# Optimization experiments

Measured on AMD Instinct MI355X. Metric: run time of the kernel, lower is better.

The kernel has to match this reference:

```python
import jax, jax.numpy as jnp
import numpy as np

N, D, H, C, E, ED, HID = 50000, 160, 5, 32, 800000, 16, 512
EPS = 1e-5  # torch LayerNorm default
NEG_SLOPE = 0.2  # GATv2Conv default negative_slope


def layer_norm(x, g, b):
    mu = x.mean(-1, keepdims=True)
    var = x.var(-1, keepdims=True)  # biased, matches torch LayerNorm
    return (x - mu) * jax.lax.rsqrt(var + EPS) * g + b


def setup_inputs() -> dict:
    key = jax.random.key(0)
    ks = jax.random.split(key, 12)
    p = lambda k, shape: jax.random.normal(k, shape, jnp.float32) * 0.05
    z = lambda *s: jnp.zeros(s, jnp.float32)
    o = lambda *s: jnp.ones(s, jnp.float32)
    return {
        "x": jax.random.normal(ks[0], (N, D), jnp.float32),
        "edge_index": jax.random.randint(ks[1], (2, E), 0, N),
        "edge_attr": jax.random.normal(ks[2], (E, ED), jnp.float32),
        "u": jax.random.normal(ks[3], (1024, 64), jnp.float32),
        "batch": jax.random.randint(ks[4], (N,), 0, 1024),
        # GATv2Conv params (lin_l, lin_r, lin_edge, att, bias)
        "Wl": p(ks[5], (D, H * C)), "bl": z(H * C),
        "Wr": p(ks[6], (D, H * C)), "br": z(H * C),
        "We": p(ks[7], (ED, H * C)),
        "att": p(ks[8], (H, C)),
        "b_gat": z(H * C),
        # norm1
        "g1": o(D), "b1": z(D),
        # output MLP: Linear(D,HID) -> SELU -> LayerNorm(HID) -> Linear(HID,D)
        "W_m1": p(ks[9], (D, HID)), "b_m1": z(HID),
        "g_m": o(HID), "b_m": z(HID),
        "W_m2": p(ks[10], (HID, D)), "b_m2": z(D),
        # norm2
        "g2": o(D), "b2": z(D),
    }


def reference(x, edge_index, edge_attr, u, batch, Wl, bl, Wr, br, We, att, b_gat,
              g1, b1, W_m1, b_m1, g_m, b_m, W_m2, b_m2, g2, b2):
    src, dst = edge_index[0], edge_index[1]  # messages flow src -> dst
    xl = (x @ Wl + bl).reshape(N, H, C)      # source projection
    xr = (x @ Wr + br).reshape(N, H, C)      # target projection
    ea = (edge_attr @ We).reshape(E, H, C)
    # GATv2 scoring: att . leaky_relu(x_l[j] + x_r[i] + e_ij)
    e = jax.nn.leaky_relu(xl[src] + xr[dst] + ea, NEG_SLOPE)   # [E,H,C]
    score = jnp.einsum('ehc,hc->eh', e, att)                   # [E,H]
    # segment softmax over incoming edges of each target node
    mx = jax.ops.segment_max(score, dst, num_segments=N)       # [N,H]
    ex = jnp.exp(score - mx[dst])
    denom = jax.ops.segment_sum(ex, dst, num_segments=N)
    alpha = ex / denom[dst]                                    # [E,H]
    agg = jax.ops.segment_sum(alpha[:, :, None] * xl[src], dst, num_segments=N)
    attn = agg.reshape(N, H * C) + b_gat                       # concat heads
    # residual + norm, MLP, residual + norm (dropout=0)
    out = layer_norm(x + attn, g1, b1)
    h = layer_norm(jax.nn.selu(out @ W_m1 + b_m1), g_m, b_m)
    mlp = h @ W_m2 + b_m2
    return layer_norm(out + mlp, g2, b2)
```

## Files before the change

kernel.cpp:

```cpp
#include <hip/hip_runtime.h>
#include <math.h>

#define N_NODES 50000
#define D 160
#define H 5
#define C 32
#define HC 160
#define E_EDGES 800000
#define ED 16
#define HID 512
#define EPS 1e-5f
#define NEG_SLOPE 0.2f

typedef __attribute__((ext_vector_type(8))) short bf16x8;
typedef __attribute__((ext_vector_type(4))) float f32x4;
typedef __attribute__((ext_vector_type(4))) short short4v;

__device__ inline float bf2f(short s) {
  unsigned u = ((unsigned)(unsigned short)s) << 16;
  return __builtin_bit_cast(float, u);
}
__device__ inline short f2bf(float f) {
  unsigned u = __builtin_bit_cast(unsigned, f);
  u = u + 0x7fffu + ((u >> 16) & 1u);
  return (short)(u >> 16);
}
__device__ inline float selu_f(float v) {
  return 1.0507009873554805f * (v > 0.f ? v : 1.6732632423543772f * (__expf(v) - 1.f));
}

__global__ void prep_weights(const float* __restrict__ Wl, const float* __restrict__ Wr,
                             const float* __restrict__ Wm1, const float* __restrict__ Wm2,
                             short* __restrict__ WlT, short* __restrict__ WrT,
                             short* __restrict__ W1T, short* __restrict__ W2T) {
  int i = blockIdx.x * blockDim.x + threadIdx.x;
  if (i < 25600) { int n = i / 160, k = i % 160; WlT[n*160 + k] = f2bf(Wl[k*160 + n]); return; }
  i -= 25600;
  if (i < 25600) { int n = i / 160, k = i % 160; WrT[n*160 + k] = f2bf(Wr[k*160 + n]); return; }
  i -= 25600;
  if (i < 81920) { int n = i / 160, k = i % 160; W1T[n*160 + k] = f2bf(Wm1[k*512 + n]); return; }
  i -= 81920;
  if (i < 81920) { int n = i / 512, k = i % 512; W2T[n*512 + k] = f2bf(Wm2[k*160 + n]); return; }
}

__global__ void convert_x(const float* __restrict__ x, short* __restrict__ xb) {
  int i = blockIdx.x * blockDim.x + threadIdx.x;
  if (i < N_NODES * D / 8) {
    const float4* s = (const float4*)(x + (size_t)i * 8);
    float4 a = s[0], b = s[1];
    bf16x8 o;
    o[0] = f2bf(a.x); o[1] = f2bf(a.y); o[2] = f2bf(a.z); o[3] = f2bf(a.w);
    o[4] = f2bf(b.x); o[5] = f2bf(b.y); o[6] = f2bf(b.z); o[7] = f2bf(b.w);
    *(bf16x8*)(xb + (size_t)i * 8) = o;
  }
}

__global__ __launch_bounds__(256) void proj_mfma(
    const short* __restrict__ xb, const short* __restrict__ WlT, const short* __restrict__ WrT,
    const float* __restrict__ bl, const float* __restrict__ br,
    short* __restrict__ xl, short* __restrict__ xr)
{
  __shared__ short As[64][40];
  int t = threadIdx.x;
  int wave = t >> 6, lane = t & 63;
  int lq = lane >> 4, lc = lane & 15;
  int row0 = blockIdx.x * 64;
  f32x4 accl[10] = {}, accr[10] = {};
  for (int kt = 0; kt < 5; ++kt) {
    int k0 = kt * 32;
    {
      int r = t >> 2, seg = t & 3;
      int gr = min(row0 + r, N_NODES - 1);
      bf16x8 v = *(const bf16x8*)&xb[(size_t)gr * 160 + k0 + seg * 8];
      *(bf16x8*)&As[r][seg * 8] = v;
    }
    __syncthreads();
    bf16x8 af = *(bf16x8*)&As[wave * 16 + lc][lq * 8];
#pragma unroll
    for (int ct = 0; ct < 10; ++ct) {
      int cc = ct * 16 + lc;
      bf16x8 bfl = *(const bf16x8*)&WlT[cc * 160 + k0 + lq * 8];
      accl[ct] = __builtin_amdgcn_mfma_f32_16x16x32_bf16(af, bfl, accl[ct], 0, 0, 0);
      bf16x8 bfr = *(const bf16x8*)&WrT[cc * 160 + k0 + lq * 8];
      accr[ct] = __builtin_amdgcn_mfma_f32_16x16x32_bf16(af, bfr, accr[ct], 0, 0, 0);
    }
    __syncthreads();
  }
#pragma unroll
  for (int ct = 0; ct < 10; ++ct) {
    int col = ct * 16 + lc;
    float bbl = bl[col], bbr = br[col];
#pragma unroll
    for (int rg = 0; rg < 4; ++rg) {
      int row = row0 + wave * 16 + lq * 4 + rg;
      if (row < N_NODES) {
        xl[(size_t)row * 160 + col] = f2bf(accl[ct][rg] + bbl);
        xr[(size_t)row * 160 + col] = f2bf(accr[ct][rg] + bbr);
      }
    }
  }
}

__global__ void count_kernel(const int* __restrict__ ei, int* __restrict__ cnt) {
  int e = blockIdx.x * blockDim.x + threadIdx.x;
  if (e < E_EDGES) atomicAdd(&cnt[ei[E_EDGES + e]], 1);
}

__global__ __launch_bounds__(1024) void scan_kernel(const int* __restrict__ cnt,
                                                    int* __restrict__ offs) {
  const int PER = (N_NODES + 1023) / 1024;
  int t = threadIdx.x;
  int start = t * PER;
  int sum = 0;
  for (int i = 0; i < PER; ++i) {
    int idx = start + i;
    if (idx < N_NODES) sum += cnt[idx];
  }
  int lane = t & 63, wid = t >> 6;
  int v = sum;
  for (int off = 1; off < 64; off <<= 1) {
    int u = __shfl_up(v, off, 64);
    if (lane >= off) v += u;
  }
  __shared__ int wsums[16];
  if (lane == 63) wsums[wid] = v;
  __syncthreads();
  if (wid == 0) {
    int w = (lane < 16) ? wsums[lane] : 0;
    for (int off = 1; off < 16; off <<= 1) {
      int u = __shfl_up(w, off, 64);
      if (lane >= off) w += u;
    }
    if (lane < 16) wsums[lane] = w;
  }
  __syncthreads();
  int excl = v - sum + (wid > 0 ? wsums[wid - 1] : 0);
  int run = excl;
  for (int i = 0; i < PER; ++i) {
    int idx = start + i;
    if (idx < N_NODES) { offs[idx] = run; run += cnt[idx]; }
  }
  if (t == 1023) offs[N_NODES] = run;
}

__global__ void scatter2(const int* __restrict__ ei, const float* __restrict__ eattr,
                         const int* __restrict__ offs, int* __restrict__ cursor,
                         int* __restrict__ srcs, short* __restrict__ eacsr) {
  int e = blockIdx.x * blockDim.x + threadIdx.x;
  if (e < E_EDGES) {
    int dst = ei[E_EDGES + e];
    int src = ei[e];
    int slot = atomicAdd(&cursor[dst], 1);
    int j = offs[dst] + slot;
    srcs[j] = src;
    const float4* s = (const float4*)&eattr[(size_t)e * ED];
    float4 v0 = s[0], v1 = s[1], v2 = s[2], v3 = s[3];
    short* o = eacsr + (size_t)j * ED;
    short4v w0, w1, w2, w3;
    w0[0]=f2bf(v0.x); w0[1]=f2bf(v0.y); w0[2]=f2bf(v0.z); w0[3]=f2bf(v0.w);
    w1[0]=f2bf(v1.x); w1[1]=f2bf(v1.y); w1[2]=f2bf(v1.z); w1[3]=f2bf(v1.w);
    w2[0]=f2bf(v2.x); w2[1]=f2bf(v2.y); w2[2]=f2bf(v2.z); w2[3]=f2bf(v2.w);
    w3[0]=f2bf(v3.x); w3[1]=f2bf(v3.y); w3[2]=f2bf(v3.z); w3[3]=f2bf(v3.w);
    *(short4v*)(o + 0) = w0; *(short4v*)(o + 4) = w1;
    *(short4v*)(o + 8) = w2; *(short4v*)(o + 12) = w3;
  }
}

__global__ __launch_bounds__(160) void attn_kernel(
    const short* __restrict__ eacsr, const int* __restrict__ srcs,
    const short* __restrict__ xl, const short* __restrict__ xr,
    const float* __restrict__ x, const float* __restrict__ We,
    const float* __restrict__ att, const float* __restrict__ b_gat,
    const float* __restrict__ g1, const float* __restrict__ b1,
    const int* __restrict__ offs,
    float* __restrict__ outb, short* __restrict__ outb_bf)
{
  __shared__ float sWe[ED][HC];
  int i = blockIdx.x;
  int t = threadIdx.x;
  for (int k = 0; k < ED; ++k) sWe[k][t] = We[k*HC + t];
  float a_t = att[t];
  float xr_t = bf2f(xr[(size_t)i*HC + t]);
  int e0 = offs[i], e1 = offs[i+1];
  __syncthreads();
  float agg = 0.f, denom = 0.f;
  for (int j = e0; j < e1; ++j) {
    int src = srcs[j];
    bf16x8 ev0 = *(const bf16x8*)&eacsr[(size_t)j*ED];
    bf16x8 ev1 = *(const bf16x8*)&eacsr[(size_t)j*ED + 8];
    float ea = 0.f;
#pragma unroll
    for (int k = 0; k < 8; ++k) ea += bf2f(ev0[k]) * sWe[k][t];
#pragma unroll
    for (int k = 0; k < 8; ++k) ea += bf2f(ev1[k]) * sWe[k+8][t];
    float xlv = bf2f(xl[(size_t)src*HC + t]);
    float v = xlv + xr_t + ea;
    v = v > 0.f ? v : NEG_SLOPE*v;
    float p = a_t * v;
#pragma unroll
    for (int m = 16; m >= 1; m >>= 1) p += __shfl_xor(p, m, 32);
    float ex = __expf(p);
    denom += ex;
    agg += ex * xlv;
  }
  float attn = (denom > 0.f) ? agg/denom : 0.f;
  float val = x[(size_t)i*HC + t] + attn + b_gat[t];
  float s1 = val, s2 = val*val;
#pragma unroll
  for (int m = 16; m >= 1; m >>= 1) { s1 += __shfl_xor(s1, m, 32); s2 += __shfl_xor(s2, m, 32); }
  __shared__ float gs1[5], gs2[5];
  __shared__ float smu, srstd;
  if ((t & 31) == 0) { gs1[t>>5] = s1; gs2[t>>5] = s2; }
  __syncthreads();
  if (t == 0) {
    float a = 0.f, b = 0.f;
    for (int g = 0; g < 5; ++g) { a += gs1[g]; b += gs2[g]; }
    float mu = a/160.f, var = b/160.f - mu*mu;
    smu = mu; srstd = rsqrtf(var + EPS);
  }
  __syncthreads();
  float o = (val - smu)*srstd*g1[t] + b1[t];
  outb[(size_t)i*HC + t] = o;
  outb_bf[(size_t)i*HC + t] = f2bf(o);
}

__global__ __launch_bounds__(256) void mlp1_mfma(
    const short* __restrict__ ab, const short* __restrict__ W1T,
    const float* __restrict__ b1m, const float* __restrict__ gm, const float* __restrict__ bm,
    short* __restrict__ h)
{
  __shared__ short As[32][40];
  __shared__ float ps1[4][32], ps2[4][32];
  int t = threadIdx.x;
  int wave = t >> 6, lane = t & 63;
  int lq = lane >> 4, lc = lane & 15;
  int row0 = blockIdx.x * 32;
  f32x4 acc[2][8] = {};
  for (int kt = 0; kt < 5; ++kt) {
    int k0 = kt * 32;
    if (t < 128) {
      int r = t >> 2, seg = t & 3;
      int gr = min(row0 + r, N_NODES - 1);
      bf16x8 v = *(const bf16x8*)&ab[(size_t)gr * 160 + k0 + seg * 8];
      *(bf16x8*)&As[r][seg * 8] = v;
    }
    __syncthreads();
    bf16x8 af0 = *(bf16x8*)&As[lc][lq * 8];
    bf16x8 af1 = *(bf16x8*)&As[16 + lc][lq * 8];
#pragma unroll
    for (int ct = 0; ct < 8; ++ct) {
      int cc = wave * 128 + ct * 16 + lc;
      bf16x8 bfv = *(const bf16x8*)&W1T[cc * 160 + k0 + lq * 8];
      acc[0][ct] = __builtin_amdgcn_mfma_f32_16x16x32_bf16(af0, bfv, acc[0][ct], 0, 0, 0);
      acc[1][ct] = __builtin_amdgcn_mfma_f32_16x16x32_bf16(af1, bfv, acc[1][ct], 0, 0, 0);
    }
    __syncthreads();
  }
  float s1[2][4] = {}, s2[2][4] = {};
#pragma unroll
  for (int rt = 0; rt < 2; ++rt)
#pragma unroll
    for (int ct = 0; ct < 8; ++ct)
#pragma unroll
      for (int rg = 0; rg < 4; ++rg) {
        int cc = wave * 128 + ct * 16 + lc;
        float v = selu_f(acc[rt][ct][rg] + b1m[cc]);
        acc[rt][ct][rg] = v;
        s1[rt][rg] += v; s2[rt][rg] += v * v;
      }
#pragma unroll
  for (int m = 1; m <= 8; m <<= 1) {
#pragma unroll
    for (int rt = 0; rt < 2; ++rt)
#pragma unroll
      for (int rg = 0; rg < 4; ++rg) {
        s1[rt][rg] += __shfl_xor(s1[rt][rg], m, 64);
        s2[rt][rg] += __shfl_xor(s2[rt][rg], m, 64);
      }
  }
  if (lc == 0) {
#pragma unroll
    for (int rt = 0; rt < 2; ++rt)
#pragma unroll
      for (int rg = 0; rg < 4; ++rg) {
        ps1[wave][rt * 16 + lq * 4 + rg] = s1[rt][rg];
        ps2[wave][rt * 16 + lq * 4 + rg] = s2[rt][rg];
      }
  }
  __syncthreads();
  float mu[2][4], rstd[2][4];
#pragma unroll
  for (int rt = 0; rt < 2; ++rt)
#pragma unroll
    for (int rg = 0; rg < 4; ++rg) {
      int rl = rt * 16 + lq * 4 + rg;
      float a = ps1[0][rl] + ps1[1][rl] + ps1[2][rl] + ps1[3][rl];
      float b = ps2[0][rl] + ps2[1][rl] + ps2[2][rl] + ps2[3][rl];
      float m_ = a * (1.f / 512.f);
      float var = b * (1.f / 512.f) - m_ * m_;
      mu[rt][rg] = m_; rstd[rt][rg] = rsqrtf(var + EPS);
    }
#pragma unroll
  for (int rt = 0; rt < 2; ++rt)
#pragma unroll
    for (int ct = 0; ct < 8; ++ct)
#pragma unroll
      for (int rg = 0; rg < 4; ++rg) {
        int row = row0 + rt * 16 + lq * 4 + rg;
        int cc = wave * 128 + ct * 16 + lc;
        if (row < N_NODES)
          h[(size_t)row * 512 + cc] =
              f2bf((acc[rt][ct][rg] - mu[rt][rg]) * rstd[rt][rg] * gm[cc] + bm[cc]);
      }
}

__global__ __launch_bounds__(256) void mlp2_mfma(
    const short* __restrict__ hb, const short* __restrict__ W2T,
    const float* __restrict__ b2m, const float* __restrict__ outb,
    const float* __restrict__ g2, const float* __restrict__ b2,
    float* __restrict__ y)
{
  __shared__ short As[64][40];
  int t = threadIdx.x;
  int wave = t >> 6, lane = t & 63;
  int lq = lane >> 4, lc = lane & 15;
  int row0 = blockIdx.x * 64;
  f32x4 acc[10] = {};
  for (int kt = 0; kt < 16; ++kt) {
    int k0 = kt * 32;
    {
      int r = t >> 2, seg = t & 3;
      int gr = min(row0 + r, N_NODES - 1);
      bf16x8 v = *(const bf16x8*)&hb[(size_t)gr * 512 + k0 + seg * 8];
      *(bf16x8*)&As[r][seg * 8] = v;
    }
    __syncthreads();
    bf16x8 af = *(bf16x8*)&As[wave * 16 + lc][lq * 8];
#pragma unroll
    for (int ct = 0; ct < 10; ++ct) {
      int cc = ct * 16 + lc;
      bf16x8 bfv = *(const bf16x8*)&W2T[cc * 512 + k0 + lq * 8];
      acc[ct] = __builtin_amdgcn_mfma_f32_16x16x32_bf16(af, bfv, acc[ct], 0, 0, 0);
    }
    __syncthreads();
  }
  float s1[4] = {}, s2[4] = {};
#pragma unroll
  for (int ct = 0; ct < 10; ++ct) {
    int col = ct * 16 + lc;
#pragma unroll
    for (int rg = 0; rg < 4; ++rg) {
      int rowl = min(row0 + wave * 16 + lq * 4 + rg, N_NODES - 1);
      float v = acc[ct][rg] + b2m[col] + outb[(size_t)rowl * 160 + col];
      acc[ct][rg] = v;
      s1[rg] += v; s2[rg] += v * v;
    }
  }
#pragma unroll
  for (int m = 1; m <= 8; m <<= 1) {
#pragma unroll
    for (int rg = 0; rg < 4; ++rg) {
      s1[rg] += __shfl_xor(s1[rg], m, 64);
      s2[rg] += __shfl_xor(s2[rg], m, 64);
    }
  }
  float mu[4], rstd[4];
#pragma unroll
  for (int rg = 0; rg < 4; ++rg) {
    float m_ = s1[rg] * (1.f / 160.f);
    float var = s2[rg] * (1.f / 160.f) - m_ * m_;
    mu[rg] = m_; rstd[rg] = rsqrtf(var + EPS);
  }
#pragma unroll
  for (int ct = 0; ct < 10; ++ct) {
    int col = ct * 16 + lc;
#pragma unroll
    for (int rg = 0; rg < 4; ++rg) {
      int row = row0 + wave * 16 + lq * 4 + rg;
      if (row < N_NODES)
        y[(size_t)row * 160 + col] = (acc[ct][rg] - mu[rg]) * rstd[rg] * g2[col] + b2[col];
    }
  }
}

extern "C" void kernel_launch(void* const* d_in, const int* in_sizes, int n_in,
                              void* d_out, int out_size, void* d_ws, size_t ws_size,
                              hipStream_t stream) {
  const float* x     = (const float*)d_in[0];
  const int*   ei    = (const int*)d_in[1];
  const float* eattr = (const float*)d_in[2];
  const float* Wl    = (const float*)d_in[5];
  const float* bl    = (const float*)d_in[6];
  const float* Wr    = (const float*)d_in[7];
  const float* br    = (const float*)d_in[8];
  const float* We    = (const float*)d_in[9];
  const float* att   = (const float*)d_in[10];
  const float* bgat  = (const float*)d_in[11];
  const float* g1    = (const float*)d_in[12];
  const float* b1    = (const float*)d_in[13];
  const float* Wm1   = (const float*)d_in[14];
  const float* bm1   = (const float*)d_in[15];
  const float* gm    = (const float*)d_in[16];
  const float* bm    = (const float*)d_in[17];
  const float* Wm2   = (const float*)d_in[18];
  const float* bm2   = (const float*)d_in[19];
  const float* g2    = (const float*)d_in[20];
  const float* b2    = (const float*)d_in[21];
  float* y = (float*)d_out;

  char* p = (char*)d_ws;
  auto alloc = [&](size_t bytes) {
    void* q = p;
    p += (bytes + 255) & ~(size_t)255;
    return q;
  };
  short* xb      = (short*)alloc((size_t)N_NODES * 160 * 2);
  short* xlb     = (short*)alloc((size_t)N_NODES * 160 * 2);
  short* xrb     = (short*)alloc((size_t)N_NODES * 160 * 2);
  float* outb    = (float*)alloc((size_t)N_NODES * 160 * 4);
  short* outb_bf = (short*)alloc((size_t)N_NODES * 160 * 2);
  short* hb      = (short*)alloc((size_t)N_NODES * 512 * 2);
  short* eacsr   = (short*)alloc((size_t)E_EDGES * 16 * 2);
  int*   srcs    = (int*)alloc((size_t)E_EDGES * 4);
  short* WlT     = (short*)alloc(160 * 160 * 2);
  short* WrT     = (short*)alloc(160 * 160 * 2);
  short* W1T     = (short*)alloc(512 * 160 * 2);
  short* W2T     = (short*)alloc(160 * 512 * 2);
  int*   cnt     = (int*)alloc((size_t)N_NODES * 4);
  int*   offs    = (int*)alloc((size_t)(N_NODES + 1) * 4);
  int*   cursor  = (int*)alloc((size_t)N_NODES * 4);

  hipMemsetAsync(cnt, 0, (size_t)N_NODES * 4, stream);
  hipMemsetAsync(cursor, 0, (size_t)N_NODES * 4, stream);

  prep_weights<<<(215040 + 255) / 256, 256, 0, stream>>>(Wl, Wr, Wm1, Wm2, WlT, WrT, W1T, W2T);
  convert_x<<<(N_NODES * 160 / 8 + 255) / 256, 256, 0, stream>>>(x, xb);
  count_kernel<<<(E_EDGES + 255) / 256, 256, 0, stream>>>(ei, cnt);
  scan_kernel<<<1, 1024, 0, stream>>>(cnt, offs);
  scatter2<<<(E_EDGES + 255) / 256, 256, 0, stream>>>(ei, eattr, offs, cursor, srcs, eacsr);
  proj_mfma<<<(N_NODES + 63) / 64, 256, 0, stream>>>(xb, WlT, WrT, bl, br, xlb, xrb);
  attn_kernel<<<N_NODES, 160, 0, stream>>>(eacsr, srcs, xlb, xrb, x, We, att, bgat,
                                           g1, b1, offs, outb, outb_bf);
  mlp1_mfma<<<(N_NODES + 31) / 32, 256, 0, stream>>>(outb_bf, W1T, bm1, gm, bm, hb);
  mlp2_mfma<<<(N_NODES + 63) / 64, 256, 0, stream>>>(hb, W2T, bm2, outb, g2, b2, y);
}
```

Before: 808.4 us.

## Split attention into edge-parallel MFMA scoring and node-wise aggregation kernels

```diff
diff --git a/kernel.cpp b/kernel.cpp
--- a/kernel.cpp
+++ b/kernel.cpp
@@ -31,8 +31,10 @@
 
 __global__ void prep_weights(const float* __restrict__ Wl, const float* __restrict__ Wr,
                              const float* __restrict__ Wm1, const float* __restrict__ Wm2,
+                             const float* __restrict__ We,
                              short* __restrict__ WlT, short* __restrict__ WrT,
-                             short* __restrict__ W1T, short* __restrict__ W2T) {
+                             short* __restrict__ W1T, short* __restrict__ W2T,
+                             short* __restrict__ WeTp) {
   int i = blockIdx.x * blockDim.x + threadIdx.x;
   if (i < 25600) { int n = i / 160, k = i % 160; WlT[n*160 + k] = f2bf(Wl[k*160 + n]); return; }
   i -= 25600;
@@ -41,6 +43,9 @@
   if (i < 81920) { int n = i / 160, k = i % 160; W1T[n*160 + k] = f2bf(Wm1[k*512 + n]); return; }
   i -= 81920;
   if (i < 81920) { int n = i / 512, k = i % 512; W2T[n*512 + k] = f2bf(Wm2[k*160 + n]); return; }
+  i -= 81920;
+  if (i < 5120) { int col = i / 32, k = i % 32;
+    WeTp[col*32 + k] = (k < ED) ? f2bf(We[k*160 + col]) : (short)0; }
 }
 
 __global__ void convert_x(const float* __restrict__ x, short* __restrict__ xb) {
@@ -143,16 +148,18 @@
   if (t == 1023) offs[N_NODES] = run;
 }
 
-__global__ void scatter2(const int* __restrict__ ei, const float* __restrict__ eattr,
+__global__ void scatter3(const int* __restrict__ ei, const float* __restrict__ eattr,
                          const int* __restrict__ offs, int* __restrict__ cursor,
-                         int* __restrict__ srcs, short* __restrict__ eacsr) {
+                         int* __restrict__ srcm, int* __restrict__ dstm,
+                         short* __restrict__ eacsr) {
   int e = blockIdx.x * blockDim.x + threadIdx.x;
   if (e < E_EDGES) {
     int dst = ei[E_EDGES + e];
     int src = ei[e];
     int slot = atomicAdd(&cursor[dst], 1);
     int j = offs[dst] + slot;
-    srcs[j] = src;
+    srcm[j] = src * 160;
+    dstm[j] = dst * 160;
     const float4* s = (const float4*)&eattr[(size_t)e * ED];
     float4 v0 = s[0], v1 = s[1], v2 = s[2], v3 = s[3];
     short* o = eacsr + (size_t)j * ED;
@@ -166,62 +173,94 @@
   }
 }
 
-__global__ __launch_bounds__(160) void attn_kernel(
-    const short* __restrict__ eacsr, const int* __restrict__ srcs,
-    const short* __restrict__ xl, const short* __restrict__ xr,
-    const float* __restrict__ x, const float* __restrict__ We,
-    const float* __restrict__ att, const float* __restrict__ b_gat,
-    const float* __restrict__ g1, const float* __restrict__ b1,
+__global__ __launch_bounds__(256) void score_mfma(
+    const short* __restrict__ eacsr, const int* __restrict__ srcm, const int* __restrict__ dstm,
+    const short* __restrict__ WeTp, const short* __restrict__ xl, const short* __restrict__ xr,
+    const float* __restrict__ att, float* __restrict__ exj)
+{
+  int t = threadIdx.x;
+  int wave = t >> 6, lane = t & 63;
+  int lq = lane >> 4, lc = lane & 15;
+  int ebase = blockIdx.x * 64 + wave * 16;
+  bf16x8 af = {};
+  if (lq < 2) af = *(const bf16x8*)&eacsr[(size_t)(ebase + lc) * ED + lq * 8];
+  f32x4 acc[10] = {};
+#pragma unroll
+  for (int ct = 0; ct < 10; ++ct) {
+    bf16x8 bfv = *(const bf16x8*)&WeTp[(ct * 16 + lc) * 32 + lq * 8];
+    acc[ct] = __builtin_amdgcn_mfma_f32_16x16x32_bf16(af, bfv, acc[ct], 0, 0, 0);
+  }
+  int srcv[4], dstv[4];
+#pragma unroll
+  for (int rg = 0; rg < 4; ++rg) {
+    int e = ebase + lq * 4 + rg;
+    srcv[rg] = srcm[e];
+    dstv[rg] = dstm[e];
+  }
+  float partial[5][4] = {};
+#pragma unroll
+  for (int ct = 0; ct < 10; ++ct) {
+    int col = ct * 16 + lc;
+    float attv = att[col];
+#pragma unroll
+    for (int rg = 0; rg < 4; ++rg) {
+      float z = acc[ct][rg] + bf2f(xl[srcv[rg] + col]) + bf2f(xr[dstv[rg] + col]);
+      z = fmaxf(z, NEG_SLOPE * z);
+      partial[ct >> 1][rg] = fmaf(z, attv, partial[ct >> 1][rg]);
+    }
+  }
+#pragma unroll
+  for (int hh = 0; hh < 5; ++hh) {
+#pragma unroll
+    for (int rg = 0; rg < 4; ++rg) {
+      float p = partial[hh][rg];
+      p += __shfl_xor(p, 1, 64);
+      p += __shfl_xor(p, 2, 64);
+      p += __shfl_xor(p, 4, 64);
+      p += __shfl_xor(p, 8, 64);
+      if (lc == hh)
+        exj[(size_t)hh * E_EDGES + (ebase + lq * 4 + rg)] = __expf(p);
+    }
+  }
+}
+
+__global__ __launch_bounds__(160) void attn_agg(
+    const int* __restrict__ srcm, const float* __restrict__ exj,
+    const short* __restrict__ xl, const float* __restrict__ x,
+    const float* __restrict__ b_gat, const float* __restrict__ g1, const float* __restrict__ b1,
     const int* __restrict__ offs,
     float* __restrict__ outb, short* __restrict__ outb_bf)
 {
-  __shared__ float sWe[ED][HC];
   int i = blockIdx.x;
   int t = threadIdx.x;
-  for (int k = 0; k < ED; ++k) sWe[k][t] = We[k*HC + t];
-  float a_t = att[t];
-  float xr_t = bf2f(xr[(size_t)i*HC + t]);
-  int e0 = offs[i], e1 = offs[i+1];
-  __syncthreads();
+  int e0 = offs[i], e1 = offs[i + 1];
+  const float* exph = exj + (size_t)(t >> 5) * E_EDGES;
   float agg = 0.f, denom = 0.f;
   for (int j = e0; j < e1; ++j) {
-    int src = srcs[j];
-    bf16x8 ev0 = *(const bf16x8*)&eacsr[(size_t)j*ED];
-    bf16x8 ev1 = *(const bf16x8*)&eacsr[(size_t)j*ED + 8];
-    float ea = 0.f;
-#pragma unroll
-    for (int k = 0; k < 8; ++k) ea += bf2f(ev0[k]) * sWe[k][t];
-#pragma unroll
-    for (int k = 0; k < 8; ++k) ea += bf2f(ev1[k]) * sWe[k+8][t];
-    float xlv = bf2f(xl[(size_t)src*HC + t]);
-    float v = xlv + xr_t + ea;
-    v = v > 0.f ? v : NEG_SLOPE*v;
-    float p = a_t * v;
-#pragma unroll
-    for (int m = 16; m >= 1; m >>= 1) p += __shfl_xor(p, m, 32);
-    float ex = __expf(p);
+    float ex = exph[j];
+    int sb = srcm[j];
+    agg = fmaf(ex, bf2f(xl[sb + t]), agg);
     denom += ex;
-    agg += ex * xlv;
-  }
-  float attn = (denom > 0.f) ? agg/denom : 0.f;
-  float val = x[(size_t)i*HC + t] + attn + b_gat[t];
-  float s1 = val, s2 = val*val;
+  }
+  float attn = (denom > 0.f) ? agg / denom : 0.f;
+  float val = x[(size_t)i * HC + t] + attn + b_gat[t];
+  float s1 = val, s2 = val * val;
 #pragma unroll
   for (int m = 16; m >= 1; m >>= 1) { s1 += __shfl_xor(s1, m, 32); s2 += __shfl_xor(s2, m, 32); }
   __shared__ float gs1[5], gs2[5];
   __shared__ float smu, srstd;
-  if ((t & 31) == 0) { gs1[t>>5] = s1; gs2[t>>5] = s2; }
+  if ((t & 31) == 0) { gs1[t >> 5] = s1; gs2[t >> 5] = s2; }
   __syncthreads();
   if (t == 0) {
     float a = 0.f, b = 0.f;
     for (int g = 0; g < 5; ++g) { a += gs1[g]; b += gs2[g]; }
-    float mu = a/160.f, var = b/160.f - mu*mu;
+    float mu = a / 160.f, var = b / 160.f - mu * mu;
     smu = mu; srstd = rsqrtf(var + EPS);
   }
   __syncthreads();
-  float o = (val - smu)*srstd*g1[t] + b1[t];
-  outb[(size_t)i*HC + t] = o;
-  outb_bf[(size_t)i*HC + t] = f2bf(o);
+  float o = (val - smu) * srstd * g1[t] + b1[t];
+  outb[(size_t)i * HC + t] = o;
+  outb_bf[(size_t)i * HC + t] = f2bf(o);
 }
 
 __global__ __launch_bounds__(256) void mlp1_mfma(
@@ -420,12 +459,15 @@
   float* outb    = (float*)alloc((size_t)N_NODES * 160 * 4);
   short* outb_bf = (short*)alloc((size_t)N_NODES * 160 * 2);
   short* hb      = (short*)alloc((size_t)N_NODES * 512 * 2);
-  short* eacsr   = (short*)alloc((size_t)E_EDGES * 16 * 2);
-  int*   srcs    = (int*)alloc((size_t)E_EDGES * 4);
+  short* eacsr   = (short*)alloc((size_t)E_EDGES * ED * 2);
+  int*   srcm    = (int*)alloc((size_t)E_EDGES * 4);
+  int*   dstm    = (int*)alloc((size_t)E_EDGES * 4);
+  float* exj     = (float*)alloc((size_t)H * E_EDGES * 4);
   short* WlT     = (short*)alloc(160 * 160 * 2);
   short* WrT     = (short*)alloc(160 * 160 * 2);
   short* W1T     = (short*)alloc(512 * 160 * 2);
   short* W2T     = (short*)alloc(160 * 512 * 2);
+  short* WeTp    = (short*)alloc(160 * 32 * 2);
   int*   cnt     = (int*)alloc((size_t)N_NODES * 4);
   int*   offs    = (int*)alloc((size_t)(N_NODES + 1) * 4);
   int*   cursor  = (int*)alloc((size_t)N_NODES * 4);
@@ -433,14 +475,16 @@
   hipMemsetAsync(cnt, 0, (size_t)N_NODES * 4, stream);
   hipMemsetAsync(cursor, 0, (size_t)N_NODES * 4, stream);
 
-  prep_weights<<<(215040 + 255) / 256, 256, 0, stream>>>(Wl, Wr, Wm1, Wm2, WlT, WrT, W1T, W2T);
+  prep_weights<<<(220160 + 255) / 256, 256, 0, stream>>>(Wl, Wr, Wm1, Wm2, We,
+                                                         WlT, WrT, W1T, W2T, WeTp);
   convert_x<<<(N_NODES * 160 / 8 + 255) / 256, 256, 0, stream>>>(x, xb);
   count_kernel<<<(E_EDGES + 255) / 256, 256, 0, stream>>>(ei, cnt);
   scan_kernel<<<1, 1024, 0, stream>>>(cnt, offs);
-  scatter2<<<(E_EDGES + 255) / 256, 256, 0, stream>>>(ei, eattr, offs, cursor, srcs, eacsr);
+  scatter3<<<(E_EDGES + 255) / 256, 256, 0, stream>>>(ei, eattr, offs, cursor,
+                                                      srcm, dstm, eacsr);
   proj_mfma<<<(N_NODES + 63) / 64, 256, 0, stream>>>(xb, WlT, WrT, bl, br, xlb, xrb);
-  attn_kernel<<<N_NODES, 160, 0, stream>>>(eacsr, srcs, xlb, xrb, x, We, att, bgat,
-                                           g1, b1, offs, outb, outb_bf);
+  score_mfma<<<E_EDGES / 64, 256, 0, stream>>>(eacsr, srcm, dstm, WeTp, xlb, xrb, att, exj);
+  attn_agg<<<N_NODES, 160, 0, stream>>>(srcm, exj, xlb, x, bgat, g1, b1, offs, outb, outb_bf);
   mlp1_mfma<<<(N_NODES + 31) / 32, 256, 0, stream>>>(outb_bf, W1T, bm1, gm, bm, hb);
   mlp2_mfma<<<(N_NODES + 63) / 64, 256, 0, stream>>>(hb, W2T, bm2, outb, g2, b2, y);
 }
```

Result: no change. 811.8 us (+0.4%).
